# Kernel optimization log

Measured on AMD Instinct MI355X. Metric: run time of the kernel, lower is better.

## Reference

```python
import jax, jax.numpy as jnp
import numpy as np

NUM_USER = 20000
NUM_ITEM = 40000
N_NODES = NUM_USER + NUM_ITEM
DIM = 64
V_DIM = 2048
T_DIM = 768
N_EDGES = 1_000_000
K_USER = 40
K_ITEM = 10
N_LAYERS = 2


def setup_inputs() -> dict:
    key = jax.random.key(0)
    ks = iter(jax.random.split(key, 32))

    def xavier(shape):
        s = (2.0 / (shape[0] + shape[-1])) ** 0.5
        return jax.random.normal(next(ks), shape, jnp.float32) * s

    # bipartite user-item interactions, doubled (undirected), as in DRAGON.__init__
    u = jax.random.randint(next(ks), (N_EDGES,), 0, NUM_USER)
    it = jax.random.randint(next(ks), (N_EDGES,), NUM_USER, N_NODES)
    edge_index = jnp.stack([jnp.concatenate([u, it]), jnp.concatenate([it, u])])

    v_feat = jax.random.normal(next(ks), (NUM_ITEM, V_DIM), jnp.float32)
    t_feat = jax.random.normal(next(ks), (NUM_ITEM, T_DIM), jnp.float32)

    # KNN item-item adjacency (top-10 per row) with symmetric-normalized values,
    # mirroring get_knn_adj_mat/compute_normalized_laplacian
    rows = jnp.repeat(jnp.arange(NUM_ITEM), K_ITEM)
    cols = jax.random.randint(next(ks), (NUM_ITEM * K_ITEM,), 0, NUM_ITEM)
    mm_indices = jnp.stack([rows, cols])
    row_sum = jax.ops.segment_sum(jnp.ones(NUM_ITEM * K_ITEM, jnp.float32), rows,
                                  num_segments=NUM_ITEM) + 1e-7
    rinv = row_sum ** -0.5
    mm_values = rinv[rows] * rinv[cols]

    user_graph = jax.random.randint(next(ks), (NUM_USER, K_USER), 0, NUM_USER)
    user_weight_matrix = jax.nn.softmax(
        jax.random.normal(next(ks), (NUM_USER, K_USER), jnp.float32), axis=1)
    weight_u = jax.nn.softmax(
        jax.random.normal(next(ks), (NUM_USER, 2, 1), jnp.float32), axis=1)

    return {
        'edge_index': edge_index,
        'v_feat': v_feat, 't_feat': t_feat,
        'v_pref': xavier((NUM_USER, DIM)), 't_pref': xavier((NUM_USER, DIM)),
        'v_mlp1_w': xavier((V_DIM, 4 * DIM)), 'v_mlp1_b': jnp.zeros(4 * DIM, jnp.float32),
        'v_mlp2_w': xavier((4 * DIM, DIM)), 'v_mlp2_b': jnp.zeros(DIM, jnp.float32),
        't_mlp1_w': xavier((T_DIM, 4 * DIM)), 't_mlp1_b': jnp.zeros(4 * DIM, jnp.float32),
        't_mlp2_w': xavier((4 * DIM, DIM)), 't_mlp2_b': jnp.zeros(DIM, jnp.float32),
        'v_conv_w': xavier((DIM, DIM)), 'v_conv_b': jnp.zeros(DIM, jnp.float32),
        't_conv_w': xavier((DIM, DIM)), 't_conv_b': jnp.zeros(DIM, jnp.float32),
        'weight_u': weight_u,
        'user_graph': user_graph,
        'user_weight_matrix': user_weight_matrix,
        'mm_indices': mm_indices,
        'mm_values': mm_values,
    }


def _l2n(x):
    n = jnp.linalg.norm(x, axis=-1, keepdims=True)
    return x / jnp.maximum(n, 1e-12)


def reference(edge_index, v_feat, t_feat, v_pref, t_pref,
              v_mlp1_w, v_mlp1_b, v_mlp2_w, v_mlp2_b,
              t_mlp1_w, t_mlp1_b, t_mlp2_w, t_mlp2_b,
              v_conv_w, v_conv_b, t_conv_w, t_conv_b,
              weight_u, user_graph, user_weight_matrix,
              mm_indices, mm_values):
    seg = jax.ops.segment_sum
    # GCNConv normalization with self-loops (shared by both branches)
    sl = jnp.arange(N_NODES)
    src = jnp.concatenate([edge_index[0], sl])
    dst = jnp.concatenate([edge_index[1], sl])
    deg = seg(jnp.ones_like(dst, dtype=jnp.float32), dst, num_segments=N_NODES)
    dinv = deg ** -0.5
    norm = (dinv[src] * dinv[dst])[:, None]

    def conv(x, w, b):  # out[dst] += norm * (x @ w)[src], then bias
        return seg(norm * (x @ w)[src], dst, num_segments=N_NODES) + b

    def branch(feat, pref, w1, b1, w2, b2, cw, cb):
        temp = jax.nn.leaky_relu(feat @ w1 + b1) @ w2 + b2  # [I, D]
        x = _l2n(jnp.concatenate([pref, temp], axis=0))      # [N, D]
        h = conv(x, cw, cb)
        h1 = conv(h, cw, cb)
        return x + h + h1

    v_rep = branch(v_feat, v_pref, v_mlp1_w, v_mlp1_b, v_mlp2_w, v_mlp2_b, v_conv_w, v_conv_b)
    t_rep = branch(t_feat, t_pref, t_mlp1_w, t_mlp1_b, t_mlp2_w, t_mlp2_b, t_conv_w, t_conv_b)

    representation = jnp.concatenate([v_rep, t_rep], axis=1)  # [N, 2D]
    wu = weight_u[:, :, 0]  # [U, 2]
    user_rep = jnp.concatenate([wu[:, 0:1] * v_rep[:NUM_USER],
                                wu[:, 1:2] * t_rep[:NUM_USER]], axis=1)  # [U, 2D]
    item_rep = representation[NUM_USER:]  # [I, 2D]

    # User_Graph_sample: weighted sum over sampled user neighborhoods
    h_u = jnp.einsum('uk,ukd->ud', user_weight_matrix, user_rep[user_graph])
    user_rep = user_rep + h_u

    # n_layers of sparse Laplacian propagation over KNN item-item graph
    row, col = mm_indices[0], mm_indices[1]
    h_i = item_rep
    for _ in range(N_LAYERS):
        h_i = seg(mm_values[:, None] * h_i[col], row, num_segments=NUM_ITEM)
    item_rep = item_rep + h_i

    return jnp.concatenate([user_rep, item_rep], axis=0)  # [N, 2D]
```

## Files before the change

kernel.cpp:

```cpp
#include <hip/hip_runtime.h>

#define NUSER 20000
#define NITEM 40000
#define NNODE 60000
#define DIM   64
#define NE    1000000
#define KUSER 40
#define KITEM 10

typedef __attribute__((ext_vector_type(8))) short short8v;
typedef __attribute__((ext_vector_type(4))) float floatx4;

__device__ inline short bf16rne(float f) {
    unsigned u = __builtin_bit_cast(unsigned, f);
    unsigned r = (u + 0x7fffu + ((u >> 16) & 1u)) >> 16;
    return (short)r;
}
__device__ inline unsigned cvt_pk_bf16(float lo, float hi) {
    unsigned r;
    asm("v_cvt_pk_bf16_f32 %0, %1, %2" : "=v"(r) : "v"(lo), "v"(hi));
    return r;
}
__device__ inline float bflo(unsigned v) { return __builtin_bit_cast(float, v << 16); }
__device__ inline float bfhi(unsigned v) { return __builtin_bit_cast(float, v & 0xffff0000u); }

__global__ __launch_bounds__(256) void k_count(const int* __restrict__ dst, int* __restrict__ cnt, int n) {
    int i = blockIdx.x * 256 + threadIdx.x;
    if (i < n) atomicAdd(&cnt[dst[i]], 1);
}

__global__ __launch_bounds__(256) void k_dinv(const int* __restrict__ cnt, float* __restrict__ dinv) {
    int i = blockIdx.x * 256 + threadIdx.x;
    if (i < NNODE) dinv[i] = 1.0f / sqrtf((float)(cnt[i] + 1));
}

__global__ __launch_bounds__(256) void k_scanA(const int* __restrict__ v, int* __restrict__ excl,
                                               int* __restrict__ bsum, int n) {
    __shared__ int s[256];
    int t = threadIdx.x, i = blockIdx.x * 256 + t;
    int orig = (i < n) ? v[i] : 0;
    s[t] = orig; __syncthreads();
    #pragma unroll
    for (int off = 1; off < 256; off <<= 1) {
        int u = (t >= off) ? s[t - off] : 0;
        __syncthreads();
        s[t] += u;
        __syncthreads();
    }
    if (i < n) excl[i] = s[t] - orig;
    if (t == 255) bsum[blockIdx.x] = s[255];
}

__global__ __launch_bounds__(256) void k_scanB(int* __restrict__ bsum, int nb) {
    __shared__ int s[256];
    int t = threadIdx.x;
    int orig = (t < nb) ? bsum[t] : 0;
    s[t] = orig; __syncthreads();
    #pragma unroll
    for (int off = 1; off < 256; off <<= 1) {
        int u = (t >= off) ? s[t - off] : 0;
        __syncthreads();
        s[t] += u;
        __syncthreads();
    }
    if (t < nb) bsum[t] = s[t] - orig;
}

__global__ __launch_bounds__(256) void k_scanC(int* __restrict__ excl, const int* __restrict__ bsum,
                                               int* __restrict__ cursor, int n) {
    int i = blockIdx.x * 256 + threadIdx.x;
    if (i < n) {
        int v = excl[i] + bsum[blockIdx.x];
        excl[i] = v;
        cursor[i] = v;
    }
    if (i == 0) excl[n] = 2 * NE;
}

__global__ __launch_bounds__(256) void k_fill(const int* __restrict__ src, const int* __restrict__ dst,
                                              const float* __restrict__ dinv, int* __restrict__ cursor,
                                              unsigned* __restrict__ csr_pkd, int n) {
    int i = blockIdx.x * 256 + threadIdx.x;
    if (i >= n) return;
    int s = src[i], d = dst[i];
    unsigned pk = ((unsigned)(unsigned short)bf16rne(dinv[s]) << 16) | (unsigned)s;
    int pos = atomicAdd(&cursor[d], 1);
    csr_pkd[pos] = pk;
}

__global__ __launch_bounds__(256) void k_transpose_bf16(const float* __restrict__ B, short* __restrict__ Btb,
                                                        int K, int N) {
    __shared__ float s[16][17];
    int t = threadIdx.x, tx = t & 15, ty = t >> 4;
    int k0 = blockIdx.x * 16, n0 = blockIdx.y * 16;
    s[ty][tx] = B[(size_t)(k0 + ty) * N + n0 + tx];
    __syncthreads();
    int k = k0 + tx, n = n0 + ty;
    Btb[(size_t)(k >> 5) * (N * 32) + n * 32 + (k & 31)] = bf16rne(s[tx][ty]);
}

__global__ __launch_bounds__(256) void k_prep(const float* __restrict__ Wv, const float* __restrict__ Wt,
                                              const float* __restrict__ bv, const float* __restrict__ bt,
                                              short* __restrict__ Bcat, float* __restrict__ bw, float* __restrict__ bb) {
    __shared__ float Wld[2][64][65];
    __shared__ float W2ld[2][64][65];
    int t = threadIdx.x;
    for (int id = t; id < 8192; id += 256) {
        int z = id >> 12, k = (id >> 6) & 63, n = id & 63;
        Wld[z][k][n] = (z ? Wt : Wv)[k * 64 + n];
    }
    __syncthreads();
    for (int id = t; id < 8192; id += 256) {
        int z = id >> 12, k = (id >> 6) & 63, n = id & 63;
        float a = 0.f;
        #pragma unroll 8
        for (int m = 0; m < 64; m++) a += Wld[z][k][m] * Wld[z][m][n];
        W2ld[z][k][n] = a;
    }
    __syncthreads();
    for (int id = t; id < 32768; id += 256) {
        int k = id >> 7, n = id & 127;
        int kb = k >> 6, kk = k & 63;
        float v = 0.f;
        if (kb == 0)      { if (n < 64)  v = Wld[0][kk][n]; }
        else if (kb == 1) { if (n >= 64) v = Wld[1][kk][n - 64]; }
        else if (kb == 2) { if (n < 64)  v = W2ld[0][kk][n]; }
        else              { if (n >= 64) v = W2ld[1][kk][n - 64]; }
        Bcat[(k >> 5) * 4096 + n * 32 + (k & 31)] = bf16rne(v);
    }
    if (t < 128) {
        int z = t >> 6, n = t & 63;
        const float* b = z ? bt : bv;
        float a = 0.f;
        #pragma unroll 8
        for (int k = 0; k < 64; k++) a += b[k] * Wld[z][k][n];
        bw[t] = a;
        bb[t] = 2.f * b[n];
    }
}

#define AP   40
#define MIDP 264
__global__ __launch_bounds__(256) void mlp_fused(const float* __restrict__ A, const short* __restrict__ B1t,
                                                 const float* __restrict__ b1, const short* __restrict__ B2t,
                                                 const float* __restrict__ b2, float* __restrict__ X,
                                                 unsigned* __restrict__ xbf, int boff, int K) {
    __shared__ short smem[2 * 64 * AP + 2 * 256 * AP];
    short* As = smem;
    short* Bs = smem + 2 * 64 * AP;
    const int tid = threadIdx.x;
    const int lane = tid & 63, wid = tid >> 6;
    const int rowBase = blockIdx.x * 64;

    const int sar = tid >> 2, sac = (tid & 3) * 8;
    const float* aptr = A + (size_t)(rowBase + sar) * K + sac;

    const int fk = (lane >> 4) * 8;
    const int faoff = (lane & 15) * AP + fk;
    const int fboff = (wid * 64 + (lane & 15)) * AP + fk;

    floatx4 acc[4][4];
    #pragma unroll
    for (int m = 0; m < 4; m++)
        #pragma unroll
        for (int n = 0; n < 4; n++) acc[m][n] = (floatx4)0.f;

    float4 ra0, ra1;
    short8v rb[4];
    const int nk = K >> 5;

    auto ldg = [&](int ks) {
        const float* ap = aptr + ks * 32;
        ra0 = *(const float4*)(ap);
        ra1 = *(const float4*)(ap + 4);
        const short* bsrc = B1t + (size_t)ks * 8192 + tid * 8;
        #pragma unroll
        for (int it = 0; it < 4; it++) rb[it] = *(const short8v*)(bsrc + it * 2048);
    };
    auto stv = [&](int buf) {
        uint4 av;
        av.x = cvt_pk_bf16(ra0.x, ra0.y); av.y = cvt_pk_bf16(ra0.z, ra0.w);
        av.z = cvt_pk_bf16(ra1.x, ra1.y); av.w = cvt_pk_bf16(ra1.z, ra1.w);
        *(uint4*)&As[buf * (64 * AP) + sar * AP + sac] = av;
        #pragma unroll
        for (int it = 0; it < 4; it++)
            *(short8v*)&Bs[buf * (256 * AP) + (sar + it * 64) * AP + sac] = rb[it];
    };

    ldg(0); stv(0);
    __syncthreads();
    int cur = 0;
    for (int ks = 0; ks < nk; ++ks) {
        if (ks + 1 < nk) ldg(ks + 1);
        short8v a[4], b[4];
        #pragma unroll
        for (int m = 0; m < 4; m++) a[m] = *(const short8v*)&As[cur * (64 * AP) + faoff + m * 16 * AP];
        #pragma unroll
        for (int n = 0; n < 4; n++) b[n] = *(const short8v*)&Bs[cur * (256 * AP) + fboff + n * 16 * AP];
        #pragma unroll
        for (int m = 0; m < 4; m++)
            #pragma unroll
            for (int n = 0; n < 4; n++)
                acc[m][n] = __builtin_amdgcn_mfma_f32_16x16x32_bf16(a[m], b[n], acc[m][n], 0, 0, 0);
        if (ks + 1 < nk) stv(cur ^ 1);
        __syncthreads();
        cur ^= 1;
    }

    short* mid = Bs;
    float bcol[4];
    #pragma unroll
    for (int n = 0; n < 4; n++) bcol[n] = b1[wid * 64 + n * 16 + (lane & 15)];
    #pragma unroll
    for (int m = 0; m < 4; m++)
        #pragma unroll
        for (int n = 0; n < 4; n++)
            #pragma unroll
            for (int q = 0; q < 4; q++) {
                int row = m * 16 + (lane >> 4) * 4 + q;
                int col = wid * 64 + n * 16 + (lane & 15);
                float v = acc[m][n][q] + bcol[n];
                v = v > 0.f ? v : 0.01f * v;
                mid[row * MIDP + col] = bf16rne(v);
            }
    __syncthreads();

    floatx4 acc2[4];
    #pragma unroll
    for (int n2 = 0; n2 < 4; n2++) acc2[n2] = (floatx4)0.f;
    const int arow = wid * 16 + (lane & 15);
    #pragma unroll
    for (int ks2 = 0; ks2 < 8; ++ks2) {
        short8v af = *(const short8v*)&mid[arow * MIDP + ks2 * 32 + fk];
        const short* bp = B2t + ks2 * 2048 + fk;
        short8v bf4[4];
        #pragma unroll
        for (int n2 = 0; n2 < 4; n2++) bf4[n2] = *(const short8v*)(bp + (n2 * 16 + (lane & 15)) * 32);
        #pragma unroll
        for (int n2 = 0; n2 < 4; n2++)
            acc2[n2] = __builtin_amdgcn_mfma_f32_16x16x32_bf16(af, bf4[n2], acc2[n2], 0, 0, 0);
    }

    float b2c[4];
    #pragma unroll
    for (int n2 = 0; n2 < 4; n2++) b2c[n2] = b2[n2 * 16 + (lane & 15)];
    #pragma unroll
    for (int q = 0; q < 4; ++q) {
        float v[4]; float ss = 0.f;
        #pragma unroll
        for (int n2 = 0; n2 < 4; n2++) { v[n2] = acc2[n2][q] + b2c[n2]; ss += v[n2] * v[n2]; }
        ss += __shfl_xor(ss, 1, 64);
        ss += __shfl_xor(ss, 2, 64);
        ss += __shfl_xor(ss, 4, 64);
        ss += __shfl_xor(ss, 8, 64);
        float sc = 1.f / fmaxf(sqrtf(ss), 1e-12f);
        int grow = rowBase + wid * 16 + (lane >> 4) * 4 + q;
        #pragma unroll
        for (int n2 = 0; n2 < 4; n2++) {
            float xn = v[n2] * sc;
            X[(size_t)grow * 64 + n2 * 16 + (lane & 15)] = xn;
            float pn = __shfl_xor(xn, 1, 64);
            if (!(lane & 1))
                xbf[(size_t)grow * 64 + boff + n2 * 8 + ((lane & 15) >> 1)] = cvt_pk_bf16(xn, pn);
        }
    }
}

__global__ __launch_bounds__(256) void k_l2n_pref(const float* __restrict__ prefv, const float* __restrict__ preft,
                                                  float* __restrict__ xv, float* __restrict__ xt,
                                                  unsigned* __restrict__ xbf) {
    int row = blockIdx.x * 4 + (threadIdx.x >> 6);
    int lane = threadIdx.x & 63;
    if (row >= NUSER) return;
    const float* p = blockIdx.y ? preft : prefv;
    float* x = blockIdx.y ? xt : xv;
    float v = p[(size_t)row * 64 + lane];
    float ss = v * v;
    #pragma unroll
    for (int off = 32; off >= 1; off >>= 1) ss += __shfl_xor(ss, off, 64);
    float xn = v / fmaxf(sqrtf(ss), 1e-12f);
    x[(size_t)row * 64 + lane] = xn;
    float pn = __shfl_xor(xn, 1, 64);
    if (!(lane & 1))
        xbf[(size_t)row * 64 + (blockIdx.y ? 32 : 0) + (lane >> 1)] = cvt_pk_bf16(xn, pn);
}

template<bool WITH_S>
__global__ __launch_bounds__(256) void k_gather_p(const int* __restrict__ rowptr, const unsigned* __restrict__ csr_pkd,
                                                  const float* __restrict__ dinv, const unsigned* __restrict__ in_bf,
                                                  unsigned* __restrict__ out_bf, float* __restrict__ s_out) {
    int row = blockIdx.x * 4 + (threadIdx.x >> 6);
    int lane = threadIdx.x & 63;
    if (row >= NNODE) return;
    int p0 = rowptr[row], p1 = rowptr[row + 1];
    float dr = dinv[row];
    unsigned sv = in_bf[(size_t)row * 64 + lane];
    float ax0 = dr * bflo(sv), ay0 = dr * bfhi(sv);
    float ax1 = 0.f, ay1 = 0.f;
    float wsum = 0.f;
    for (int p = p0; p < p1; p += 64) {
        int c = p1 - p; if (c > 64) c = 64;
        unsigned pk = (lane < c) ? csr_pkd[p + lane] : 0u;
        if (WITH_S) wsum += bfhi(pk);
        int j = 0;
        for (; j + 4 <= c; j += 4) {
            unsigned e0 = __shfl(pk, j, 64),     e1 = __shfl(pk, j + 1, 64);
            unsigned e2 = __shfl(pk, j + 2, 64), e3 = __shfl(pk, j + 3, 64);
            unsigned v0 = in_bf[(size_t)(e0 & 0xffffu) * 64 + lane];
            unsigned v1 = in_bf[(size_t)(e1 & 0xffffu) * 64 + lane];
            unsigned v2 = in_bf[(size_t)(e2 & 0xffffu) * 64 + lane];
            unsigned v3 = in_bf[(size_t)(e3 & 0xffffu) * 64 + lane];
            float w0 = bfhi(e0), w1 = bfhi(e1), w2 = bfhi(e2), w3 = bfhi(e3);
            ax0 += w0 * bflo(v0); ay0 += w0 * bfhi(v0);
            ax1 += w1 * bflo(v1); ay1 += w1 * bfhi(v1);
            ax0 += w2 * bflo(v2); ay0 += w2 * bfhi(v2);
            ax1 += w3 * bflo(v3); ay1 += w3 * bfhi(v3);
        }
        for (; j < c; ++j) {
            unsigned e = __shfl(pk, j, 64);
            unsigned v = in_bf[(size_t)(e & 0xffffu) * 64 + lane];
            float w = bfhi(e);
            ax0 += w * bflo(v); ay0 += w * bfhi(v);
        }
    }
    out_bf[(size_t)row * 64 + lane] = cvt_pk_bf16(dr * (ax0 + ax1), dr * (ay0 + ay1));
    if (WITH_S) {
        #pragma unroll
        for (int o = 32; o >= 1; o >>= 1) wsum += __shfl_xor(wsum, o, 64);
        if (lane == 0) s_out[row] = dr * (dr + wsum);
    }
}

__global__ __launch_bounds__(256) void k_rep_gemm(const unsigned* __restrict__ g1, const unsigned* __restrict__ g2,
                                                  const short* __restrict__ Bcat,
                                                  const float* __restrict__ xv, const float* __restrict__ xt,
                                                  const float* __restrict__ s, const float* __restrict__ bw,
                                                  const float* __restrict__ bb, const float* __restrict__ weight_u,
                                                  float* __restrict__ rep0, unsigned* __restrict__ rep_bf) {
    __shared__ short Alds[64 * 264];
    const int tid = threadIdx.x, lane = tid & 63, wid = tid >> 6;
    const int rowBase = blockIdx.x * 64;
    #pragma unroll
    for (int i = 0; i < 8; i++) {
        int cid = tid + i * 256;
        int r = cid >> 5, c = cid & 31;
        int grow = rowBase + r; if (grow >= NNODE) grow = NNODE - 1;
        const unsigned* src = (c < 16) ? (g1 + (size_t)grow * 64 + c * 4)
                                       : (g2 + (size_t)grow * 64 + (c - 16) * 4);
        uint4 v = *(const uint4*)src;
        *(uint4*)&Alds[r * 264 + c * 8] = v;
    }
    __syncthreads();
    const int fk = (lane >> 4) * 8;
    const int arow = wid * 16 + (lane & 15);
    floatx4 acc[8];
    #pragma unroll
    for (int n = 0; n < 8; n++) acc[n] = (floatx4)0.f;
    #pragma unroll
    for (int ks = 0; ks < 8; ks++) {
        short8v af = *(const short8v*)&Alds[arow * 264 + ks * 32 + fk];
        #pragma unroll
        for (int n = 0; n < 8; n++) {
            short8v bf = *(const short8v*)(Bcat + ks * 4096 + (n * 16 + (lane & 15)) * 32 + fk);
            acc[n] = __builtin_amdgcn_mfma_f32_16x16x32_bf16(af, bf, acc[n], 0, 0, 0);
        }
    }
    #pragma unroll
    for (int n = 0; n < 8; n++) {
        int col = n * 16 + (lane & 15);
        float bwc = bw[col], bbc = bb[col];
        #pragma unroll
        for (int q = 0; q < 4; q++) {
            int row = rowBase + wid * 16 + (lane >> 4) * 4 + q;
            int rc = row < NNODE ? row : NNODE - 1;
            float xval = (col < 64) ? xv[(size_t)rc * 64 + col] : xt[(size_t)rc * 64 + col - 64];
            float v = acc[n][q] + xval + s[rc] * bwc + bbc;
            float w = (rc < NUSER) ? weight_u[rc * 2 + (col >> 6)] : 1.0f;
            v *= w;
            float pn = __shfl_xor(v, 1, 64);
            if (row < NNODE) {
                rep0[(size_t)row * 128 + col] = v;
                if (!(lane & 1))
                    rep_bf[(size_t)row * 64 + n * 8 + ((lane & 15) >> 1)] = cvt_pk_bf16(v, pn);
            }
        }
    }
}

#define UBLK (NUSER * 64 / 256)
__global__ __launch_bounds__(256) void k_user_item1(const float* __restrict__ rep0, const unsigned* __restrict__ rep_bf,
                                                    const int* __restrict__ ug, const float* __restrict__ uwm,
                                                    const int* __restrict__ mm_col, const float* __restrict__ mm_values,
                                                    float* __restrict__ out, unsigned* __restrict__ tmp_bf) {
    int bid = blockIdx.x;
    if (bid < UBLK) {
        int id = bid * 256 + threadIdx.x;
        int u = id >> 6, lane = id & 63;
        float2 acc = *(const float2*)(rep0 + (size_t)u * 128 + 2 * lane);
        #pragma unroll 4
        for (int k = 0; k < KUSER; k++) {
            int nb = ug[u * KUSER + k];
            float w = uwm[u * KUSER + k];
            unsigned v = rep_bf[(size_t)nb * 64 + lane];
            acc.x += w * bflo(v);
            acc.y += w * bfhi(v);
        }
        *(float2*)(out + (size_t)u * 128 + 2 * lane) = acc;
    } else {
        int id = (bid - UBLK) * 256 + threadIdx.x;
        int r = id >> 6, lane = id & 63;
        float ax = 0.f, ay = 0.f;
        #pragma unroll
        for (int j = 0; j < KITEM; j++) {
            int c = mm_col[r * KITEM + j];
            float w = mm_values[r * KITEM + j];
            unsigned v = rep_bf[(size_t)(NUSER + c) * 64 + lane];
            ax += w * bflo(v);
            ay += w * bfhi(v);
        }
        tmp_bf[(size_t)r * 64 + lane] = cvt_pk_bf16(ax, ay);
    }
}

__global__ __launch_bounds__(256) void k_item2(const float* __restrict__ rep0, const unsigned* __restrict__ tmp_bf,
                                               const int* __restrict__ mm_col, const float* __restrict__ mm_values,
                                               float* __restrict__ out) {
    int id = blockIdx.x * 256 + threadIdx.x;
    int r = id >> 6, lane = id & 63;
    if (r >= NITEM) return;
    float ax = 0.f, ay = 0.f;
    #pragma unroll
    for (int j = 0; j < KITEM; j++) {
        int c = mm_col[r * KITEM + j];
        float w = mm_values[r * KITEM + j];
        unsigned v = tmp_bf[(size_t)c * 64 + lane];
        ax += w * bflo(v);
        ay += w * bfhi(v);
    }
    float2 base = *(const float2*)(rep0 + (size_t)(NUSER + r) * 128 + 2 * lane);
    float2 o;
    o.x = base.x + ax;
    o.y = base.y + ay;
    *(float2*)(out + (size_t)(NUSER + r) * 128 + 2 * lane) = o;
}

extern "C" void kernel_launch(void* const* d_in, const int* in_sizes, int n_in,
                              void* d_out, int out_size, void* d_ws, size_t ws_size,
                              hipStream_t stream) {
    const int*   edge_index = (const int*)d_in[0];
    const float* v_feat   = (const float*)d_in[1];
    const float* t_feat   = (const float*)d_in[2];
    const float* v_pref   = (const float*)d_in[3];
    const float* t_pref   = (const float*)d_in[4];
    const float* v_mlp1_w = (const float*)d_in[5];
    const float* v_mlp1_b = (const float*)d_in[6];
    const float* v_mlp2_w = (const float*)d_in[7];
    const float* v_mlp2_b = (const float*)d_in[8];
    const float* t_mlp1_w = (const float*)d_in[9];
    const float* t_mlp1_b = (const float*)d_in[10];
    const float* t_mlp2_w = (const float*)d_in[11];
    const float* t_mlp2_b = (const float*)d_in[12];
    const float* v_conv_w = (const float*)d_in[13];
    const float* v_conv_b = (const float*)d_in[14];
    const float* t_conv_w = (const float*)d_in[15];
    const float* t_conv_b = (const float*)d_in[16];
    const float* weight_u = (const float*)d_in[17];
    const int*   user_graph = (const int*)d_in[18];
    const float* uwm      = (const float*)d_in[19];
    const int*   mm_indices = (const int*)d_in[20];
    const float* mm_values  = (const float*)d_in[21];
    float* out = (float*)d_out;

    char* wsb = (char*)d_ws;
    size_t off = 0;
    auto alloc = [&](size_t bytes) -> void* {
        void* p = wsb + off;
        off = (off + bytes + 255) & ~(size_t)255;
        return p;
    };
    int*      cnt     = (int*)     alloc(NNODE * 4);
    float*    dinv    = (float*)   alloc(NNODE * 4);
    int*      rowptr  = (int*)     alloc((NNODE + 1) * 4);
    int*      bsum    = (int*)     alloc(256 * 4);
    int*      cursor  = (int*)     alloc(NNODE * 4);
    unsigned* csr_pkd = (unsigned*)alloc((size_t)2 * NE * 4);
    short*    Btw     = (short*)   alloc((size_t)2048 * 256 * 2);
    short*    W2b     = (short*)   alloc((size_t)256 * 64 * 2);
    short*    Bcat    = (short*)   alloc((size_t)256 * 128 * 2);
    float*    bw      = (float*)   alloc(128 * 4);
    float*    bb      = (float*)   alloc(128 * 4);
    float*    svec    = (float*)   alloc(NNODE * 4);
    float*    xv      = (float*)   alloc((size_t)NNODE * DIM * 4);
    float*    xt      = (float*)   alloc((size_t)NNODE * DIM * 4);
    unsigned* x_bf    = (unsigned*)alloc((size_t)NNODE * 64 * 4);
    unsigned* g1      = (unsigned*)alloc((size_t)NNODE * 64 * 4);
    unsigned* g2      = (unsigned*)alloc((size_t)NNODE * 64 * 4);
    float*    rep0    = (float*)   alloc((size_t)NNODE * 128 * 4);
    unsigned* rep_bf  = (unsigned*)alloc((size_t)NNODE * 64 * 4);
    unsigned* tmp_bf  = (unsigned*)alloc((size_t)NITEM * 64 * 4);
    (void)ws_size; (void)n_in; (void)in_sizes; (void)out_size;

    const int* e_src = edge_index;
    const int* e_dst = edge_index + 2 * NE;
    const int* mm_col = mm_indices + NITEM * KITEM;

    const int NB = (NNODE + 255) / 256;

    hipMemsetAsync(cnt, 0, NNODE * 4, stream);
    k_count<<<(2 * NE + 255) / 256, 256, 0, stream>>>(e_dst, cnt, 2 * NE);
    k_dinv<<<(NNODE + 255) / 256, 256, 0, stream>>>(cnt, dinv);
    k_scanA<<<NB, 256, 0, stream>>>(cnt, rowptr, bsum, NNODE);
    k_scanB<<<1, 256, 0, stream>>>(bsum, NB);
    k_scanC<<<NB, 256, 0, stream>>>(rowptr, bsum, cursor, NNODE);
    k_fill<<<(2 * NE + 255) / 256, 256, 0, stream>>>(e_src, e_dst, dinv, cursor, csr_pkd, 2 * NE);

    k_prep<<<1, 256, 0, stream>>>(v_conv_w, t_conv_w, v_conv_b, t_conv_b, Bcat, bw, bb);

    {
        dim3 t1(2048 / 16, 16);
        k_transpose_bf16<<<t1, 256, 0, stream>>>(v_mlp1_w, Btw, 2048, 256);
        dim3 t2(256 / 16, 4);
        k_transpose_bf16<<<t2, 256, 0, stream>>>(v_mlp2_w, W2b, 256, 64);
        mlp_fused<<<NITEM / 64, 256, 0, stream>>>(v_feat, Btw, v_mlp1_b, W2b, v_mlp2_b,
                                                  xv + (size_t)NUSER * DIM, x_bf + (size_t)NUSER * 64, 0, 2048);
        dim3 t3(768 / 16, 16);
        k_transpose_bf16<<<t3, 256, 0, stream>>>(t_mlp1_w, Btw, 768, 256);
        k_transpose_bf16<<<t2, 256, 0, stream>>>(t_mlp2_w, W2b, 256, 64);
        mlp_fused<<<NITEM / 64, 256, 0, stream>>>(t_feat, Btw, t_mlp1_b, W2b, t_mlp2_b,
                                                  xt + (size_t)NUSER * DIM, x_bf + (size_t)NUSER * 64, 32, 768);
    }
    {
        dim3 g(NUSER / 4, 2);
        k_l2n_pref<<<g, 256, 0, stream>>>(v_pref, t_pref, xv, xt, x_bf);
    }

    k_gather_p<true><<<(NNODE + 3) / 4, 256, 0, stream>>>(rowptr, csr_pkd, dinv, x_bf, g1, svec);
    k_gather_p<false><<<(NNODE + 3) / 4, 256, 0, stream>>>(rowptr, csr_pkd, dinv, g1, g2, nullptr);
    k_rep_gemm<<<(NNODE + 63) / 64, 256, 0, stream>>>(g1, g2, Bcat, xv, xt, svec, bw, bb, weight_u,
                                                      rep0, rep_bf);

    k_user_item1<<<UBLK + NITEM * 64 / 256, 256, 0, stream>>>(rep0, rep_bf, user_graph, uwm,
                                                              mm_col, mm_values, out, tmp_bf);
    k_item2<<<NITEM * 64 / 256, 256, 0, stream>>>(rep0, tmp_bf, mm_col, mm_values, out);
}
```

Before: 627.4 us.

## Fuse second graph gather into rep GEMM, drop fp32 x buffers and LDS B staging

Result: no change. 617.4 us (-1.6%).

```diff
diff --git a/kernel.cpp b/kernel.cpp
--- a/kernel.cpp
+++ b/kernel.cpp
@@ -143,11 +143,10 @@
 #define MIDP 264
 __global__ __launch_bounds__(256) void mlp_fused(const float* __restrict__ A, const short* __restrict__ B1t,
                                                  const float* __restrict__ b1, const short* __restrict__ B2t,
-                                                 const float* __restrict__ b2, float* __restrict__ X,
+                                                 const float* __restrict__ b2,
                                                  unsigned* __restrict__ xbf, int boff, int K) {
-    __shared__ short smem[2 * 64 * AP + 2 * 256 * AP];
+    __shared__ short smem[64 * MIDP];
     short* As = smem;
-    short* Bs = smem + 2 * 64 * AP;
     const int tid = threadIdx.x;
     const int lane = tid & 63, wid = tid >> 6;
     const int rowBase = blockIdx.x * 64;
@@ -157,7 +156,7 @@
 
     const int fk = (lane >> 4) * 8;
     const int faoff = (lane & 15) * AP + fk;
-    const int fboff = (wid * 64 + (lane & 15)) * AP + fk;
+    const int bcol0 = wid * 64 + (lane & 15);
 
     floatx4 acc[4][4];
     #pragma unroll
@@ -166,25 +165,18 @@
         for (int n = 0; n < 4; n++) acc[m][n] = (floatx4)0.f;
 
     float4 ra0, ra1;
-    short8v rb[4];
     const int nk = K >> 5;
 
     auto ldg = [&](int ks) {
         const float* ap = aptr + ks * 32;
         ra0 = *(const float4*)(ap);
         ra1 = *(const float4*)(ap + 4);
-        const short* bsrc = B1t + (size_t)ks * 8192 + tid * 8;
-        #pragma unroll
-        for (int it = 0; it < 4; it++) rb[it] = *(const short8v*)(bsrc + it * 2048);
     };
     auto stv = [&](int buf) {
         uint4 av;
         av.x = cvt_pk_bf16(ra0.x, ra0.y); av.y = cvt_pk_bf16(ra0.z, ra0.w);
         av.z = cvt_pk_bf16(ra1.x, ra1.y); av.w = cvt_pk_bf16(ra1.z, ra1.w);
         *(uint4*)&As[buf * (64 * AP) + sar * AP + sac] = av;
-        #pragma unroll
-        for (int it = 0; it < 4; it++)
-            *(short8v*)&Bs[buf * (256 * AP) + (sar + it * 64) * AP + sac] = rb[it];
     };
 
     ldg(0); stv(0);
@@ -194,9 +186,10 @@
         if (ks + 1 < nk) ldg(ks + 1);
         short8v a[4], b[4];
         #pragma unroll
+        for (int n = 0; n < 4; n++)
+            b[n] = *(const short8v*)(B1t + (size_t)ks * 8192 + (bcol0 + n * 16) * 32 + fk);
+        #pragma unroll
         for (int m = 0; m < 4; m++) a[m] = *(const short8v*)&As[cur * (64 * AP) + faoff + m * 16 * AP];
-        #pragma unroll
-        for (int n = 0; n < 4; n++) b[n] = *(const short8v*)&Bs[cur * (256 * AP) + fboff + n * 16 * AP];
         #pragma unroll
         for (int m = 0; m < 4; m++)
             #pragma unroll
@@ -207,7 +200,7 @@
         cur ^= 1;
     }
 
-    short* mid = Bs;
+    short* mid = smem;
     float bcol[4];
     #pragma unroll
     for (int n = 0; n < 4; n++) bcol[n] = b1[wid * 64 + n * 16 + (lane & 15)];
@@ -258,7 +251,6 @@
         #pragma unroll
         for (int n2 = 0; n2 < 4; n2++) {
             float xn = v[n2] * sc;
-            X[(size_t)grow * 64 + n2 * 16 + (lane & 15)] = xn;
             float pn = __shfl_xor(xn, 1, 64);
             if (!(lane & 1))
                 xbf[(size_t)grow * 64 + boff + n2 * 8 + ((lane & 15) >> 1)] = cvt_pk_bf16(xn, pn);
@@ -267,25 +259,21 @@
 }
 
 __global__ __launch_bounds__(256) void k_l2n_pref(const float* __restrict__ prefv, const float* __restrict__ preft,
-                                                  float* __restrict__ xv, float* __restrict__ xt,
                                                   unsigned* __restrict__ xbf) {
     int row = blockIdx.x * 4 + (threadIdx.x >> 6);
     int lane = threadIdx.x & 63;
     if (row >= NUSER) return;
     const float* p = blockIdx.y ? preft : prefv;
-    float* x = blockIdx.y ? xt : xv;
     float v = p[(size_t)row * 64 + lane];
     float ss = v * v;
     #pragma unroll
     for (int off = 32; off >= 1; off >>= 1) ss += __shfl_xor(ss, off, 64);
     float xn = v / fmaxf(sqrtf(ss), 1e-12f);
-    x[(size_t)row * 64 + lane] = xn;
     float pn = __shfl_xor(xn, 1, 64);
     if (!(lane & 1))
         xbf[(size_t)row * 64 + (blockIdx.y ? 32 : 0) + (lane >> 1)] = cvt_pk_bf16(xn, pn);
 }
 
-template<bool WITH_S>
 __global__ __launch_bounds__(256) void k_gather_p(const int* __restrict__ rowptr, const unsigned* __restrict__ csr_pkd,
                                                   const float* __restrict__ dinv, const unsigned* __restrict__ in_bf,
                                                   unsigned* __restrict__ out_bf, float* __restrict__ s_out) {
@@ -301,7 +289,7 @@
     for (int p = p0; p < p1; p += 64) {
         int c = p1 - p; if (c > 64) c = 64;
         unsigned pk = (lane < c) ? csr_pkd[p + lane] : 0u;
-        if (WITH_S) wsum += bfhi(pk);
+        wsum += bfhi(pk);
         int j = 0;
         for (; j + 4 <= c; j += 4) {
             unsigned e0 = __shfl(pk, j, 64),     e1 = __shfl(pk, j + 1, 64);
@@ -324,66 +312,81 @@
         }
     }
     out_bf[(size_t)row * 64 + lane] = cvt_pk_bf16(dr * (ax0 + ax1), dr * (ay0 + ay1));
-    if (WITH_S) {
-        #pragma unroll
-        for (int o = 32; o >= 1; o >>= 1) wsum += __shfl_xor(wsum, o, 64);
-        if (lane == 0) s_out[row] = dr * (dr + wsum);
-    }
-}
-
-__global__ __launch_bounds__(256) void k_rep_gemm(const unsigned* __restrict__ g1, const unsigned* __restrict__ g2,
-                                                  const short* __restrict__ Bcat,
-                                                  const float* __restrict__ xv, const float* __restrict__ xt,
-                                                  const float* __restrict__ s, const float* __restrict__ bw,
-                                                  const float* __restrict__ bb, const float* __restrict__ weight_u,
-                                                  float* __restrict__ rep0, unsigned* __restrict__ rep_bf) {
-    __shared__ short Alds[64 * 264];
-    const int tid = threadIdx.x, lane = tid & 63, wid = tid >> 6;
-    const int rowBase = blockIdx.x * 64;
-    #pragma unroll
-    for (int i = 0; i < 8; i++) {
-        int cid = tid + i * 256;
-        int r = cid >> 5, c = cid & 31;
-        int grow = rowBase + r; if (grow >= NNODE) grow = NNODE - 1;
-        const unsigned* src = (c < 16) ? (g1 + (size_t)grow * 64 + c * 4)
-                                       : (g2 + (size_t)grow * 64 + (c - 16) * 4);
-        uint4 v = *(const uint4*)src;
-        *(uint4*)&Alds[r * 264 + c * 8] = v;
-    }
-    __syncthreads();
-    const int fk = (lane >> 4) * 8;
-    const int arow = wid * 16 + (lane & 15);
-    floatx4 acc[8];
-    #pragma unroll
-    for (int n = 0; n < 8; n++) acc[n] = (floatx4)0.f;
-    #pragma unroll
-    for (int ks = 0; ks < 8; ks++) {
-        short8v af = *(const short8v*)&Alds[arow * 264 + ks * 32 + fk];
-        #pragma unroll
-        for (int n = 0; n < 8; n++) {
-            short8v bf = *(const short8v*)(Bcat + ks * 4096 + (n * 16 + (lane & 15)) * 32 + fk);
-            acc[n] = __builtin_amdgcn_mfma_f32_16x16x32_bf16(af, bf, acc[n], 0, 0, 0);
-        }
-    }
-    #pragma unroll
-    for (int n = 0; n < 8; n++) {
-        int col = n * 16 + (lane & 15);
-        float bwc = bw[col], bbc = bb[col];
-        #pragma unroll
-        for (int q = 0; q < 4; q++) {
-            int row = rowBase + wid * 16 + (lane >> 4) * 4 + q;
-            int rc = row < NNODE ? row : NNODE - 1;
-            float xval = (col < 64) ? xv[(size_t)rc * 64 + col] : xt[(size_t)rc * 64 + col - 64];
-            float v = acc[n][q] + xval + s[rc] * bwc + bbc;
-            float w = (rc < NUSER) ? weight_u[rc * 2 + (col >> 6)] : 1.0f;
-            v *= w;
-            float pn = __shfl_xor(v, 1, 64);
-            if (row < NNODE) {
-                rep0[(size_t)row * 128 + col] = v;
-                if (!(lane & 1))
-                    rep_bf[(size_t)row * 64 + n * 8 + ((lane & 15) >> 1)] = cvt_pk_bf16(v, pn);
+    #pragma unroll
+    for (int o = 32; o >= 1; o >>= 1) wsum += __shfl_xor(wsum, o, 64);
+    if (lane == 0) s_out[row] = dr * (dr + wsum);
+}
+
+__global__ __launch_bounds__(512) void k_gather2_rep(const int* __restrict__ rowptr, const unsigned* __restrict__ csr_pkd,
+                                                     const float* __restrict__ dinv, const unsigned* __restrict__ g1,
+                                                     const short* __restrict__ Bcat, const unsigned* __restrict__ x_bf,
+                                                     const float* __restrict__ s, const float* __restrict__ bw,
+                                                     const float* __restrict__ bb, const float* __restrict__ weight_u,
+                                                     float* __restrict__ rep0, unsigned* __restrict__ rep_bf) {
+    __shared__ short As[16 * 264];
+    const int tid = threadIdx.x, lane = tid & 63, w = tid >> 6;
+    const int rowBase = blockIdx.x * 16;
+
+    for (int rr = 0; rr < 2; ++rr) {
+        int lrow = w * 2 + rr;
+        int row = rowBase + lrow;
+        int p0 = rowptr[row], p1 = rowptr[row + 1];
+        float dr = dinv[row];
+        unsigned sv = g1[(size_t)row * 64 + lane];
+        float ax0 = dr * bflo(sv), ay0 = dr * bfhi(sv);
+        float ax1 = 0.f, ay1 = 0.f;
+        for (int p = p0; p < p1; p += 64) {
+            int c = p1 - p; if (c > 64) c = 64;
+            unsigned pk = (lane < c) ? csr_pkd[p + lane] : 0u;
+            int j = 0;
+            for (; j + 4 <= c; j += 4) {
+                unsigned e0 = __shfl(pk, j, 64),     e1 = __shfl(pk, j + 1, 64);
+                unsigned e2 = __shfl(pk, j + 2, 64), e3 = __shfl(pk, j + 3, 64);
+                unsigned v0 = g1[(size_t)(e0 & 0xffffu) * 64 + lane];
+                unsigned v1 = g1[(size_t)(e1 & 0xffffu) * 64 + lane];
+                unsigned v2 = g1[(size_t)(e2 & 0xffffu) * 64 + lane];
+                unsigned v3 = g1[(size_t)(e3 & 0xffffu) * 64 + lane];
+                float w0 = bfhi(e0), w1 = bfhi(e1), w2 = bfhi(e2), w3 = bfhi(e3);
+                ax0 += w0 * bflo(v0); ay0 += w0 * bfhi(v0);
+                ax1 += w1 * bflo(v1); ay1 += w1 * bfhi(v1);
+                ax0 += w2 * bflo(v2); ay0 += w2 * bfhi(v2);
+                ax1 += w3 * bflo(v3); ay1 += w3 * bfhi(v3);
+            }
+            for (; j < c; ++j) {
+                unsigned e = __shfl(pk, j, 64);
+                unsigned v = g1[(size_t)(e & 0xffffu) * 64 + lane];
+                float wj = bfhi(e);
+                ax0 += wj * bflo(v); ay0 += wj * bfhi(v);
             }
         }
+        *(unsigned*)&As[lrow * 264 + 2 * lane] = sv;
+        *(unsigned*)&As[lrow * 264 + 128 + 2 * lane] = cvt_pk_bf16(dr * (ax0 + ax1), dr * (ay0 + ay1));
+    }
+    __syncthreads();
+
+    const int fk = (lane >> 4) * 8;
+    floatx4 acc = (floatx4)0.f;
+    #pragma unroll
+    for (int ks = 0; ks < 8; ++ks) {
+        short8v af = *(const short8v*)&As[(lane & 15) * 264 + ks * 32 + fk];
+        short8v bf = *(const short8v*)(Bcat + ks * 4096 + (w * 16 + (lane & 15)) * 32 + fk);
+        acc = __builtin_amdgcn_mfma_f32_16x16x32_bf16(af, bf, acc, 0, 0, 0);
+    }
+    const int col = w * 16 + (lane & 15);
+    const float bwc = bw[col], bbc = bb[col];
+    #pragma unroll
+    for (int q = 0; q < 4; ++q) {
+        int lrow = (lane >> 4) * 4 + q;
+        int row = rowBase + lrow;
+        unsigned xw = x_bf[(size_t)row * 64 + (col >> 1)];
+        float xval = (col & 1) ? bfhi(xw) : bflo(xw);
+        float v = acc[q] + xval + s[row] * bwc + bbc;
+        float wu = (row < NUSER) ? weight_u[row * 2 + (col >> 6)] : 1.0f;
+        v *= wu;
+        rep0[(size_t)row * 128 + col] = v;
+        float pn = __shfl_xor(v, 1, 64);
+        if (!(lane & 1))
+            rep_bf[(size_t)row * 64 + (col >> 1)] = cvt_pk_bf16(v, pn);
     }
 }
 
@@ -490,11 +493,8 @@
     float*    bw      = (float*)   alloc(128 * 4);
     float*    bb      = (float*)   alloc(128 * 4);
     float*    svec    = (float*)   alloc(NNODE * 4);
-    float*    xv      = (float*)   alloc((size_t)NNODE * DIM * 4);
-    float*    xt      = (float*)   alloc((size_t)NNODE * DIM * 4);
     unsigned* x_bf    = (unsigned*)alloc((size_t)NNODE * 64 * 4);
     unsigned* g1      = (unsigned*)alloc((size_t)NNODE * 64 * 4);
-    unsigned* g2      = (unsigned*)alloc((size_t)NNODE * 64 * 4);
     float*    rep0    = (float*)   alloc((size_t)NNODE * 128 * 4);
     unsigned* rep_bf  = (unsigned*)alloc((size_t)NNODE * 64 * 4);
     unsigned* tmp_bf  = (unsigned*)alloc((size_t)NITEM * 64 * 4);
@@ -522,22 +522,21 @@
         dim3 t2(256 / 16, 4);
         k_transpose_bf16<<<t2, 256, 0, stream>>>(v_mlp2_w, W2b, 256, 64);
         mlp_fused<<<NITEM / 64, 256, 0, stream>>>(v_feat, Btw, v_mlp1_b, W2b, v_mlp2_b,
-                                                  xv + (size_t)NUSER * DIM, x_bf + (size_t)NUSER * 64, 0, 2048);
+                                                  x_bf + (size_t)NUSER * 64, 0, 2048);
         dim3 t3(768 / 16, 16);
         k_transpose_bf16<<<t3, 256, 0, stream>>>(t_mlp1_w, Btw, 768, 256);
         k_transpose_bf16<<<t2, 256, 0, stream>>>(t_mlp2_w, W2b, 256, 64);
         mlp_fused<<<NITEM / 64, 256, 0, stream>>>(t_feat, Btw, t_mlp1_b, W2b, t_mlp2_b,
-                                                  xt + (size_t)NUSER * DIM, x_bf + (size_t)NUSER * 64, 32, 768);
+                                                  x_bf + (size_t)NUSER * 64, 32, 768);
     }
     {
         dim3 g(NUSER / 4, 2);
-        k_l2n_pref<<<g, 256, 0, stream>>>(v_pref, t_pref, xv, xt, x_bf);
-    }
-
-    k_gather_p<true><<<(NNODE + 3) / 4, 256, 0, stream>>>(rowptr, csr_pkd, dinv, x_bf, g1, svec);
-    k_gather_p<false><<<(NNODE + 3) / 4, 256, 0, stream>>>(rowptr, csr_pkd, dinv, g1, g2, nullptr);
-    k_rep_gemm<<<(NNODE + 63) / 64, 256, 0, stream>>>(g1, g2, Bcat, xv, xt, svec, bw, bb, weight_u,
-                                                      rep0, rep_bf);
+        k_l2n_pref<<<g, 256, 0, stream>>>(v_pref, t_pref, x_bf);
+    }
+
+    k_gather_p<<<(NNODE + 3) / 4, 256, 0, stream>>>(rowptr, csr_pkd, dinv, x_bf, g1, svec);
+    k_gather2_rep<<<NNODE / 16, 512, 0, stream>>>(rowptr, csr_pkd, dinv, g1, Bcat, x_bf,
+                                                  svec, bw, bb, weight_u, rep0, rep_bf);
 
     k_user_item1<<<UBLK + NITEM * 64 / 256, 256, 0, stream>>>(rep0, rep_bf, user_graph, uwm,
                                                               mm_col, mm_values, out, tmp_bf);
```
